# Kernel optimization log

Hardware: AMD Instinct MI355X
Metric: run time of the kernel (lower is better)

## Reference

```python
import jax, jax.numpy as jnp
import numpy as np

N_HEADS = 16
HEAD_DIM = 64
HIDDEN = N_HEADS * HEAD_DIM


def setup_inputs() -> dict:
    key = jax.random.key(0)
    ks = jax.random.split(key, 10)
    B, F, T = 2, 2048, 2048
    std = 0.02
    inp = {
        "from_tensor": jax.random.normal(ks[0], (B, F, HIDDEN), dtype=jnp.float32),
        "to_tensor": jax.random.normal(ks[1], (B, T, HIDDEN), dtype=jnp.float32),
        "attention_mask": jax.random.randint(ks[2], (B, F, T), 0, 2, dtype=jnp.int32),
        "Wq": jax.random.normal(ks[3], (HIDDEN, HIDDEN), dtype=jnp.float32) * std,
        "bq": jnp.zeros((HIDDEN,), dtype=jnp.float32),
        "Wk": jax.random.normal(ks[4], (HIDDEN, HIDDEN), dtype=jnp.float32) * std,
        "bk": jnp.zeros((HIDDEN,), dtype=jnp.float32),
        "Wv": jax.random.normal(ks[5], (HIDDEN, HIDDEN), dtype=jnp.float32) * std,
        "bv": jnp.zeros((HIDDEN,), dtype=jnp.float32),
    }
    return inp


def reference(from_tensor, to_tensor, attention_mask, Wq, bq, Wk, bk, Wv, bv):
    B, F, _ = from_tensor.shape
    T = to_tensor.shape[1]
    N, H = N_HEADS, HEAD_DIM

    # QKV projections (no activations: query/key/value act fns are None)
    q = (from_tensor @ Wq + bq).reshape(B, F, N, H)
    k = (to_tensor @ Wk + bk).reshape(B, T, N, H)
    v = (to_tensor @ Wv + bv).reshape(B, T, N, H)

    scores = jnp.einsum('BFNH,BTNH->BNFT', q, k) * (1.0 / np.sqrt(float(H)))
    # additive mask: mask [B,F,T] -> [B,1,F,T]; 0 entries get -10000
    adder = (1.0 - attention_mask.astype(jnp.float32))[:, None, :, :] * -10000.0
    scores = scores + adder
    probs = jax.nn.softmax(scores, axis=-1)  # dropout skipped (inference)

    context = jnp.einsum('BNFT,BTNH->BFNH', probs, v)
    return context.reshape(B, F, N * H)
```

## Files before the change

### kernel.cpp

```cpp
#include <hip/hip_runtime.h>


typedef short v8s __attribute__((ext_vector_type(8)));
typedef float v4f __attribute__((ext_vector_type(4)));
typedef unsigned short u16;
typedef unsigned int   u32;
typedef unsigned long long u64;

constexpr float QSCALE = 0.18033688011112042f;

__device__ __forceinline__ u16 f2bf(float f) {
    u32 u = __builtin_bit_cast(u32, f);
    u += 0x7fffu + ((u >> 16) & 1u);
    return (u16)(u >> 16);
}

__device__ __forceinline__ u32 pack_bf16(float a, float b) {
    u32 ua = __builtin_bit_cast(u32, a);
    u32 ub = __builtin_bit_cast(u32, b);
    ua += 0x7fffu + ((ua >> 16) & 1u);
    ub += 0x7fffu + ((ub >> 16) & 1u);
    return (ua >> 16) | (ub & 0xffff0000u);
}

__device__ __forceinline__ v8s ld8(const u16* p) {
    return *reinterpret_cast<const v8s*>(p);
}

__device__ __forceinline__ void async16(const void* g, void* l) {
    __builtin_amdgcn_global_load_lds(
        (const __attribute__((address_space(1))) u32*)g,
        (__attribute__((address_space(3))) u32*)l, 16, 0, 0);
}

__global__ void cvt_bf16_2(const float* __restrict__ a, const float* __restrict__ bsrc,
                           u16* __restrict__ da, u16* __restrict__ db, int n4) {
    int i = blockIdx.x * blockDim.x + threadIdx.x;
    const float4* s;
    ushort4* d;
    int j;
    if (i < n4) { s = (const float4*)a;    d = (ushort4*)da; j = i; }
    else        { s = (const float4*)bsrc; d = (ushort4*)db; j = i - n4; }
    float4 v = s[j];
    ushort4 o;
    o.x = f2bf(v.x); o.y = f2bf(v.y); o.z = f2bf(v.z); o.w = f2bf(v.w);
    d[j] = o;
}

__global__ void transpose_w(const float* __restrict__ Wq, const float* __restrict__ Wk,
                            const float* __restrict__ Wv,
                            u16* __restrict__ Wqt, u16* __restrict__ Wkt, u16* __restrict__ Wvt) {
    __shared__ float tile[32][33];
    const float* W = blockIdx.z == 0 ? Wq : (blockIdx.z == 1 ? Wk : Wv);
    u16* Wt = blockIdx.z == 0 ? Wqt : (blockIdx.z == 1 ? Wkt : Wvt);
    const int tx = threadIdx.x, ty = threadIdx.y;
    const int n0 = blockIdx.x * 32, k0 = blockIdx.y * 32;
    for (int i = 0; i < 4; i++)
        tile[ty + i * 8][tx] = W[(size_t)(k0 + ty + i * 8) * 1024 + n0 + tx];
    __syncthreads();
    for (int i = 0; i < 4; i++)
        Wt[(size_t)(n0 + ty + i * 8) * 1024 + k0 + tx] = f2bf(tile[tx][ty + i * 8]);
}

__global__ void mask_pack(const int* __restrict__ mask, u64* __restrict__ words, int nwords) {
    int g = blockIdx.x * blockDim.x + threadIdx.x;
    int w = g >> 6, lane = g & 63;
    if (w < nwords) {
        int v = mask[(size_t)w * 64 + lane];
        u64 bits = __ballot(v != 0);
        if (lane == 0) words[w] = bits;
    }
}

__global__ __launch_bounds__(256) void gemm_qkv(
    const u16* __restrict__ Xf, const u16* __restrict__ Xt,
    const u16* __restrict__ Wqt, const u16* __restrict__ Wkt, const u16* __restrict__ Wvt,
    const float* __restrict__ bq, const float* __restrict__ bk, const float* __restrict__ bv,
    u16* __restrict__ Qb, u16* __restrict__ Kb, u16* __restrict__ Vtb) {
    const int z = blockIdx.z;
    const u16* A      = z == 0 ? Xf : Xt;
    const u16* Bt     = z == 0 ? Wqt : (z == 1 ? Wkt : Wvt);
    const float* bias = z == 0 ? bq : (z == 1 ? bk : bv);
    u16* C            = z == 0 ? Qb : (z == 1 ? Kb : Vtb);
    const int mode    = (z == 2);
    const float sc    = (z == 0) ? QSCALE : 1.0f;

    __shared__ u16 As[128 * 32];
    __shared__ u16 Bs[128 * 32];
    const uint4* Ag = reinterpret_cast<const uint4*>(A);
    const uint4* Bg = reinterpret_cast<const uint4*>(Bt);

    const int tid = threadIdx.x;
    const int lane = tid & 63, wave = tid >> 6;
    const int quad = lane >> 4, l16 = lane & 15;
    const int wm = wave >> 1, wn = wave & 1;
    const int m0 = blockIdx.x * 128, n0 = blockIdx.y * 128;

    const int cg  = (lane & 3) ^ ((lane >> 3) & 3);
    const int sw8 = (quad ^ ((l16 >> 1) & 3)) * 8;

    const int r0 = (wave * 2 + 0) * 16 + (lane >> 2);
    const int r1 = (wave * 2 + 1) * 16 + (lane >> 2);
    const uint4* ap0 = Ag + (size_t)(m0 + r0) * 128 + cg;
    const uint4* ap1 = Ag + (size_t)(m0 + r1) * 128 + cg;
    const uint4* bp0 = Bg + (size_t)(n0 + r0) * 128 + cg;
    const uint4* bp1 = Bg + (size_t)(n0 + r1) * 128 + cg;

    v4f acc[4][4];
    for (int i = 0; i < 4; i++)
        for (int j = 0; j < 4; j++) acc[i][j] = (v4f)0.0f;

    for (int k0 = 0; k0 < 32; k0++) {
        __syncthreads();
        async16(ap0, As + (wave * 2 + 0) * 512); ap0 += 4;
        async16(ap1, As + (wave * 2 + 1) * 512); ap1 += 4;
        async16(bp0, Bs + (wave * 2 + 0) * 512); bp0 += 4;
        async16(bp1, Bs + (wave * 2 + 1) * 512); bp1 += 4;
        __syncthreads();

        v8s af[4], bf[4];
        #pragma unroll
        for (int mt = 0; mt < 4; mt++) af[mt] = ld8(&As[(wm * 64 + mt * 16 + l16) * 32 + sw8]);
        #pragma unroll
        for (int nt = 0; nt < 4; nt++) bf[nt] = ld8(&Bs[(wn * 64 + nt * 16 + l16) * 32 + sw8]);
        #pragma unroll
        for (int mt = 0; mt < 4; mt++)
            #pragma unroll
            for (int nt = 0; nt < 4; nt++)
                acc[mt][nt] = __builtin_amdgcn_mfma_f32_16x16x32_bf16(af[mt], bf[nt], acc[mt][nt], 0, 0, 0);
    }

    #pragma unroll
    for (int nt = 0; nt < 4; nt++) {
        const int col = n0 + wn * 64 + nt * 16 + l16;
        const float bvv = bias[col];
        #pragma unroll
        for (int mt = 0; mt < 4; mt++) {
            const int mbase = m0 + wm * 64 + mt * 16 + quad * 4;
            if (mode == 0) {
                for (int r = 0; r < 4; r++)
                    C[(size_t)(mbase + r) * 1024 + col] = f2bf((acc[mt][nt][r] + bvv) * sc);
            } else {
                const int b = mbase >> 11, t = mbase & 2047;
                const int head = col >> 6, h = col & 63;
                ushort4 pk;
                pk.x = f2bf(acc[mt][nt][0] + bvv);
                pk.y = f2bf(acc[mt][nt][1] + bvv);
                pk.z = f2bf(acc[mt][nt][2] + bvv);
                pk.w = f2bf(acc[mt][nt][3] + bvv);
                *reinterpret_cast<ushort4*>(&C[(size_t)((b * 16 + head) * 64 + h) * 2048 + t]) = pk;
            }
        }
    }
}

__global__ __launch_bounds__(256, 2) void attn_fused(
    const u16* __restrict__ Qb, const u16* __restrict__ Kb,
    const u16* __restrict__ Vtb, const u64* __restrict__ mw,
    float* __restrict__ out) {
    __shared__ u16 Ks[2][2][64][32];
    __shared__ u16 Vs[2][2][64][32];
    __shared__ u32 Ps[4][32 * 36];

    const int tid = threadIdx.x;
    const int lane = tid & 63, wave = tid >> 6;
    const int quad = lane >> 4, l16 = lane & 15;
    const int b = blockIdx.x >> 4, head = blockIdx.x & 15;
    const int f0 = blockIdx.y * 128;

    const uint4* Kg = reinterpret_cast<const uint4*>(Kb);
    const uint4* Vg = reinterpret_cast<const uint4*>(Vtb);
    const size_t vbase4 = (size_t)(b * 16 + head) * 64 * 256;

    const int cg  = (lane & 3) ^ ((lane >> 3) & 3);
    const int sw8 = (quad ^ ((l16 >> 1) & 3)) * 8;

    v8s qf[2][2];
    #pragma unroll
    for (int kk = 0; kk < 2; kk++)
        #pragma unroll
        for (int qh = 0; qh < 2; qh++)
            qf[kk][qh] = ld8(Qb + ((size_t)(b * 2048 + f0 + wave * 32 + qh * 16 + l16) * 16 + head) * 64
                                + kk * 32 + quad * 8);

    const int kr0 = ((wave * 2 + 0) * 64 + lane) >> 2;
    const int kr1 = ((wave * 2 + 1) * 64 + lane) >> 2;
    const uint4* kp0 = Kg + ((size_t)(b * 2048 + (kr0 & 63)) * 16 + head) * 8 + (kr0 >> 6) * 4 + cg;
    const uint4* kp1 = Kg + ((size_t)(b * 2048 + (kr1 & 63)) * 16 + head) * 8 + (kr1 >> 6) * 4 + cg;
    const uint4* vp0 = Vg + vbase4 + (size_t)(kr0 & 63) * 256 + (kr0 >> 6) * 4 + cg;
    const uint4* vp1 = Vg + vbase4 + (size_t)(kr1 & 63) * 256 + (kr1 >> 6) * 4 + cg;
    const int dK0 = (wave * 2 + 0) * 512, dK1 = (wave * 2 + 1) * 512;

    float lsum[2] = {0.f, 0.f};
    v4f accO[2][4];
    #pragma unroll
    for (int qh = 0; qh < 2; qh++)
        for (int ht = 0; ht < 4; ht++) accO[qh][ht] = (v4f)0.0f;

    u32* myPs = Ps[wave];
    const u64* mrow = mw + (size_t)(b * 2048 + f0 + wave * 32 + l16) * 32;

    async16(kp0, (u16*)Ks + dK0); kp0 += 8192;
    async16(kp1, (u16*)Ks + dK1); kp1 += 8192;
    async16(vp0, (u16*)Vs + dK0); vp0 += 8;
    async16(vp1, (u16*)Vs + dK1); vp1 += 8;
    __syncthreads();

    for (int it = 0; it < 32; it++) {
        const int cur = it & 1, nxt = cur ^ 1;
        if (it < 31) {
            async16(kp0, (u16*)Ks + nxt * 4096 + dK0); kp0 += 8192;
            async16(kp1, (u16*)Ks + nxt * 4096 + dK1); kp1 += 8192;
            async16(vp0, (u16*)Vs + nxt * 4096 + dK0); vp0 += 8;
            async16(vp1, (u16*)Vs + nxt * 4096 + dK1); vp1 += 8;
        }

        v4f s[2][4];
        #pragma unroll
        for (int qh = 0; qh < 2; qh++)
            for (int mt = 0; mt < 4; mt++) s[qh][mt] = (v4f)0.0f;
        #pragma unroll
        for (int kk = 0; kk < 2; kk++) {
            v8s kf[4];
            #pragma unroll
            for (int mt = 0; mt < 4; mt++) kf[mt] = ld8(&Ks[cur][kk][mt * 16 + l16][sw8]);
            #pragma unroll
            for (int qh = 0; qh < 2; qh++)
                #pragma unroll
                for (int mt = 0; mt < 4; mt++)
                    s[qh][mt] = __builtin_amdgcn_mfma_f32_16x16x32_bf16(kf[mt], qf[kk][qh], s[qh][mt], 0, 0, 0);
        }

        u32 pk[2][8];
        #pragma unroll
        for (int qh = 0; qh < 2; qh++) {
            const u64 w = mrow[qh * 512 + it];
            const u32 lo = (u32)(w >> (quad * 4));
            const u32 hi = (u32)(w >> (quad * 4 + 32));
            float sum = 0.f;
            #pragma unroll
            for (int mt = 0; mt < 4; mt++) {
                const u32 bits = ((mt & 2) ? hi : lo) >> ((mt & 1) * 16);
                float p[4];
                #pragma unroll
                for (int r = 0; r < 4; r++) {
                    const float e = __builtin_amdgcn_exp2f(s[qh][mt][r]);
                    p[r] = ((bits >> r) & 1u) ? e : 0.0f;
                    sum += p[r];
                }
                pk[qh][mt * 2]     = pack_bf16(p[0], p[1]);
                pk[qh][mt * 2 + 1] = pack_bf16(p[2], p[3]);
            }
            lsum[qh] += sum;
        }

        #pragma unroll
        for (int qh = 0; qh < 2; qh++) {
            const int row = qh * 16 + l16;
            #pragma unroll
            for (int mt = 0; mt < 4; mt++)
                *reinterpret_cast<uint2*>(&myPs[row * 36 + mt * 8 + quad * 2]) =
                    make_uint2(pk[qh][mt * 2], pk[qh][mt * 2 + 1]);
        }

        #pragma unroll
        for (int kk = 0; kk < 2; kk++) {
            v8s vf[4];
            #pragma unroll
            for (int ht = 0; ht < 4; ht++) vf[ht] = ld8(&Vs[cur][kk][ht * 16 + l16][sw8]);
            #pragma unroll
            for (int qh = 0; qh < 2; qh++) {
                const v8s pf = *reinterpret_cast<const v8s*>(
                    &myPs[(qh * 16 + l16) * 36 + kk * 16 + quad * 4]);
                #pragma unroll
                for (int ht = 0; ht < 4; ht++)
                    accO[qh][ht] = __builtin_amdgcn_mfma_f32_16x16x32_bf16(vf[ht], pf, accO[qh][ht], 0, 0, 0);
            }
        }

        __syncthreads();
    }

    #pragma unroll
    for (int qh = 0; qh < 2; qh++) {
        float l = lsum[qh];
        l += __shfl_xor(l, 16);
        l += __shfl_xor(l, 32);
        const float inv = 1.0f / l;
        const size_t ro = (size_t)(b * 2048 + f0 + wave * 32 + qh * 16 + l16) * 1024 + head * 64;
        #pragma unroll
        for (int ht = 0; ht < 4; ht++) {
            float4 o;
            o.x = accO[qh][ht][0] * inv;
            o.y = accO[qh][ht][1] * inv;
            o.z = accO[qh][ht][2] * inv;
            o.w = accO[qh][ht][3] * inv;
            *reinterpret_cast<float4*>(&out[ro + ht * 16 + quad * 4]) = o;
        }
    }
}

extern "C" void kernel_launch(void* const* d_in, const int* in_sizes, int n_in,
                              void* d_out, int out_size, void* d_ws, size_t ws_size,
                              hipStream_t stream) {
    const float* from = (const float*)d_in[0];
    const float* to   = (const float*)d_in[1];
    const int*   mask = (const int*)d_in[2];
    const float* Wq = (const float*)d_in[3];
    const float* bq = (const float*)d_in[4];
    const float* Wk = (const float*)d_in[5];
    const float* bk = (const float*)d_in[6];
    const float* Wv = (const float*)d_in[7];
    const float* bv = (const float*)d_in[8];
    float* out = (float*)d_out;

    u16* Xf  = (u16*)d_ws;
    u16* Xt  = Xf  + 4194304;
    u16* Wqt = Xt  + 4194304;
    u16* Wkt = Wqt + 1048576;
    u16* Wvt = Wkt + 1048576;
    u16* Qb  = Wvt + 1048576;
    u16* Kb  = Qb  + 4194304;
    u16* Vtb = Kb  + 4194304;
    u64* mwords = (u64*)(Vtb + 4194304);

    cvt_bf16_2<<<8192, 256, 0, stream>>>(from, to, Xf, Xt, 1048576);
    transpose_w<<<dim3(32, 32, 3), dim3(32, 8), 0, stream>>>(Wq, Wk, Wv, Wqt, Wkt, Wvt);
    mask_pack<<<32768, 256, 0, stream>>>(mask, mwords, 131072);

    gemm_qkv<<<dim3(32, 8, 3), 256, 0, stream>>>(Xf, Xt, Wqt, Wkt, Wvt, bq, bk, bv, Qb, Kb, Vtb);

    attn_fused<<<dim3(32, 16), 256, 0, stream>>>(Qb, Kb, Vtb, mwords, out);
}
```

Measured before the change: 251.6 us.

## Split attention over two key halves, merge prep kernels, add reduction pass

Merges the three preprocessing kernels into one launch. The attention kernel now splits the key dimension into two halves across a grid z-dimension, which doubles the block count, and raises launch bounds to 4 blocks per CU. It does this by dropping double buffering to a single buffer with two syncs per iteration. Row sums are computed with an extra MFMA against a ones vector instead of scalar adds, and P is truncated rather than rounded to bf16. A new reduce kernel combines the two partial outputs, reusing workspace for the second half (it overwrites the Xf/Xt staging buffers and the transposed weights). This adds extra global traffic and loses load/compute overlap.

```diff
diff --git a/kernel.cpp b/kernel.cpp
--- a/kernel.cpp
+++ b/kernel.cpp
@@ -15,11 +15,9 @@
     return (u16)(u >> 16);
 }
 
-__device__ __forceinline__ u32 pack_bf16(float a, float b) {
+__device__ __forceinline__ u32 pack_trunc(float a, float b) {
     u32 ua = __builtin_bit_cast(u32, a);
     u32 ub = __builtin_bit_cast(u32, b);
-    ua += 0x7fffu + ((ua >> 16) & 1u);
-    ub += 0x7fffu + ((ub >> 16) & 1u);
     return (ua >> 16) | (ub & 0xffff0000u);
 }
 
@@ -33,39 +31,40 @@
         (__attribute__((address_space(3))) u32*)l, 16, 0, 0);
 }
 
-__global__ void cvt_bf16_2(const float* __restrict__ a, const float* __restrict__ bsrc,
-                           u16* __restrict__ da, u16* __restrict__ db, int n4) {
-    int i = blockIdx.x * blockDim.x + threadIdx.x;
-    const float4* s;
-    ushort4* d;
-    int j;
-    if (i < n4) { s = (const float4*)a;    d = (ushort4*)da; j = i; }
-    else        { s = (const float4*)bsrc; d = (ushort4*)db; j = i - n4; }
-    float4 v = s[j];
-    ushort4 o;
-    o.x = f2bf(v.x); o.y = f2bf(v.y); o.z = f2bf(v.z); o.w = f2bf(v.w);
-    d[j] = o;
-}
-
-__global__ void transpose_w(const float* __restrict__ Wq, const float* __restrict__ Wk,
-                            const float* __restrict__ Wv,
-                            u16* __restrict__ Wqt, u16* __restrict__ Wkt, u16* __restrict__ Wvt) {
+__global__ __launch_bounds__(256) void prep(
+    const float* __restrict__ from, const float* __restrict__ to,
+    u16* __restrict__ Xf, u16* __restrict__ Xt,
+    const float* __restrict__ Wq, const float* __restrict__ Wk, const float* __restrict__ Wv,
+    u16* __restrict__ Wqt, u16* __restrict__ Wkt, u16* __restrict__ Wvt,
+    const int* __restrict__ mask, u64* __restrict__ words) {
     __shared__ float tile[32][33];
-    const float* W = blockIdx.z == 0 ? Wq : (blockIdx.z == 1 ? Wk : Wv);
-    u16* Wt = blockIdx.z == 0 ? Wqt : (blockIdx.z == 1 ? Wkt : Wvt);
-    const int tx = threadIdx.x, ty = threadIdx.y;
-    const int n0 = blockIdx.x * 32, k0 = blockIdx.y * 32;
-    for (int i = 0; i < 4; i++)
-        tile[ty + i * 8][tx] = W[(size_t)(k0 + ty + i * 8) * 1024 + n0 + tx];
-    __syncthreads();
-    for (int i = 0; i < 4; i++)
-        Wt[(size_t)(n0 + ty + i * 8) * 1024 + k0 + tx] = f2bf(tile[tx][ty + i * 8]);
-}
-
-__global__ void mask_pack(const int* __restrict__ mask, u64* __restrict__ words, int nwords) {
-    int g = blockIdx.x * blockDim.x + threadIdx.x;
-    int w = g >> 6, lane = g & 63;
-    if (w < nwords) {
+    const int bid = blockIdx.x, tid = threadIdx.x;
+    if (bid < 8192) {
+        int i = bid * 256 + tid;
+        const float4* s;
+        ushort4* d;
+        int j;
+        if (i < 1048576) { s = (const float4*)from; d = (ushort4*)Xf; j = i; }
+        else             { s = (const float4*)to;   d = (ushort4*)Xt; j = i - 1048576; }
+        float4 v = s[j];
+        ushort4 o;
+        o.x = f2bf(v.x); o.y = f2bf(v.y); o.z = f2bf(v.z); o.w = f2bf(v.w);
+        d[j] = o;
+    } else if (bid < 11264) {
+        const int r = bid - 8192;
+        const int zz = r >> 10, rem = r & 1023;
+        const float* W = zz == 0 ? Wq : (zz == 1 ? Wk : Wv);
+        u16* Wt = zz == 0 ? Wqt : (zz == 1 ? Wkt : Wvt);
+        const int tx = tid & 31, ty = tid >> 5;
+        const int n0 = (rem & 31) * 32, k0 = (rem >> 5) * 32;
+        for (int i = 0; i < 4; i++)
+            tile[ty + i * 8][tx] = W[(size_t)(k0 + ty + i * 8) * 1024 + n0 + tx];
+        __syncthreads();
+        for (int i = 0; i < 4; i++)
+            Wt[(size_t)(n0 + ty + i * 8) * 1024 + k0 + tx] = f2bf(tile[tx][ty + i * 8]);
+    } else {
+        int g = (bid - 11264) * 256 + tid;
+        int w = g >> 6, lane = g & 63;
         int v = mask[(size_t)w * 64 + lane];
         u64 bits = __ballot(v != 0);
         if (lane == 0) words[w] = bits;
@@ -154,12 +153,13 @@
     }
 }
 
-__global__ __launch_bounds__(256, 2) void attn_fused(
+__global__ __launch_bounds__(256, 4) void attn_fused(
     const u16* __restrict__ Qb, const u16* __restrict__ Kb,
     const u16* __restrict__ Vtb, const u64* __restrict__ mw,
-    float* __restrict__ out) {
-    __shared__ u16 Ks[2][2][64][32];
-    __shared__ u16 Vs[2][2][64][32];
+    float* __restrict__ out, float* __restrict__ O1,
+    float* __restrict__ l0w, float* __restrict__ l1w) {
+    __shared__ u16 Ks[2][64][32];
+    __shared__ u16 Vs[2][64][32];
     __shared__ u32 Ps[4][32 * 36];
 
     const int tid = threadIdx.x;
@@ -167,6 +167,8 @@
     const int quad = lane >> 4, l16 = lane & 15;
     const int b = blockIdx.x >> 4, head = blockIdx.x & 15;
     const int f0 = blockIdx.y * 128;
+    const int thalf = blockIdx.z;
+    const int tbase = thalf * 1024;
 
     const uint4* Kg = reinterpret_cast<const uint4*>(Kb);
     const uint4* Vg = reinterpret_cast<const uint4*>(Vtb);
@@ -183,37 +185,35 @@
             qf[kk][qh] = ld8(Qb + ((size_t)(b * 2048 + f0 + wave * 32 + qh * 16 + l16) * 16 + head) * 64
                                 + kk * 32 + quad * 8);
 
+    v8s ones;
+    #pragma unroll
+    for (int i = 0; i < 8; i++) ones[i] = (short)0x3F80;
+
     const int kr0 = ((wave * 2 + 0) * 64 + lane) >> 2;
     const int kr1 = ((wave * 2 + 1) * 64 + lane) >> 2;
-    const uint4* kp0 = Kg + ((size_t)(b * 2048 + (kr0 & 63)) * 16 + head) * 8 + (kr0 >> 6) * 4 + cg;
-    const uint4* kp1 = Kg + ((size_t)(b * 2048 + (kr1 & 63)) * 16 + head) * 8 + (kr1 >> 6) * 4 + cg;
-    const uint4* vp0 = Vg + vbase4 + (size_t)(kr0 & 63) * 256 + (kr0 >> 6) * 4 + cg;
-    const uint4* vp1 = Vg + vbase4 + (size_t)(kr1 & 63) * 256 + (kr1 >> 6) * 4 + cg;
+    const uint4* kp0 = Kg + ((size_t)(b * 2048 + tbase + (kr0 & 63)) * 16 + head) * 8 + (kr0 >> 6) * 4 + cg;
+    const uint4* kp1 = Kg + ((size_t)(b * 2048 + tbase + (kr1 & 63)) * 16 + head) * 8 + (kr1 >> 6) * 4 + cg;
+    const uint4* vp0 = Vg + vbase4 + (size_t)(kr0 & 63) * 256 + (tbase >> 3) + (kr0 >> 6) * 4 + cg;
+    const uint4* vp1 = Vg + vbase4 + (size_t)(kr1 & 63) * 256 + (tbase >> 3) + (kr1 >> 6) * 4 + cg;
     const int dK0 = (wave * 2 + 0) * 512, dK1 = (wave * 2 + 1) * 512;
 
-    float lsum[2] = {0.f, 0.f};
-    v4f accO[2][4];
-    #pragma unroll
-    for (int qh = 0; qh < 2; qh++)
+    v4f accO[2][4], accL[2];
+    #pragma unroll
+    for (int qh = 0; qh < 2; qh++) {
+        accL[qh] = (v4f)0.0f;
         for (int ht = 0; ht < 4; ht++) accO[qh][ht] = (v4f)0.0f;
+    }
 
     u32* myPs = Ps[wave];
-    const u64* mrow = mw + (size_t)(b * 2048 + f0 + wave * 32 + l16) * 32;
-
-    async16(kp0, (u16*)Ks + dK0); kp0 += 8192;
-    async16(kp1, (u16*)Ks + dK1); kp1 += 8192;
-    async16(vp0, (u16*)Vs + dK0); vp0 += 8;
-    async16(vp1, (u16*)Vs + dK1); vp1 += 8;
-    __syncthreads();
-
-    for (int it = 0; it < 32; it++) {
-        const int cur = it & 1, nxt = cur ^ 1;
-        if (it < 31) {
-            async16(kp0, (u16*)Ks + nxt * 4096 + dK0); kp0 += 8192;
-            async16(kp1, (u16*)Ks + nxt * 4096 + dK1); kp1 += 8192;
-            async16(vp0, (u16*)Vs + nxt * 4096 + dK0); vp0 += 8;
-            async16(vp1, (u16*)Vs + nxt * 4096 + dK1); vp1 += 8;
-        }
+    const u64* mrow = mw + (size_t)(b * 2048 + f0 + wave * 32 + l16) * 32 + thalf * 16;
+
+    for (int it = 0; it < 16; it++) {
+        __syncthreads();
+        async16(kp0, (u16*)Ks + dK0); kp0 += 8192;
+        async16(kp1, (u16*)Ks + dK1); kp1 += 8192;
+        async16(vp0, (u16*)Vs + dK0); vp0 += 8;
+        async16(vp1, (u16*)Vs + dK1); vp1 += 8;
+        __syncthreads();
 
         v4f s[2][4];
         #pragma unroll
@@ -223,7 +223,7 @@
         for (int kk = 0; kk < 2; kk++) {
             v8s kf[4];
             #pragma unroll
-            for (int mt = 0; mt < 4; mt++) kf[mt] = ld8(&Ks[cur][kk][mt * 16 + l16][sw8]);
+            for (int mt = 0; mt < 4; mt++) kf[mt] = ld8(&Ks[kk][mt * 16 + l16][sw8]);
             #pragma unroll
             for (int qh = 0; qh < 2; qh++)
                 #pragma unroll
@@ -237,7 +237,6 @@
             const u64 w = mrow[qh * 512 + it];
             const u32 lo = (u32)(w >> (quad * 4));
             const u32 hi = (u32)(w >> (quad * 4 + 32));
-            float sum = 0.f;
             #pragma unroll
             for (int mt = 0; mt < 4; mt++) {
                 const u32 bits = ((mt & 2) ? hi : lo) >> ((mt & 1) * 16);
@@ -246,12 +245,10 @@
                 for (int r = 0; r < 4; r++) {
                     const float e = __builtin_amdgcn_exp2f(s[qh][mt][r]);
                     p[r] = ((bits >> r) & 1u) ? e : 0.0f;
-                    sum += p[r];
                 }
-                pk[qh][mt * 2]     = pack_bf16(p[0], p[1]);
-                pk[qh][mt * 2 + 1] = pack_bf16(p[2], p[3]);
+                pk[qh][mt * 2]     = pack_trunc(p[0], p[1]);
+                pk[qh][mt * 2 + 1] = pack_trunc(p[2], p[3]);
             }
-            lsum[qh] += sum;
         }
 
         #pragma unroll
@@ -267,7 +264,7 @@
         for (int kk = 0; kk < 2; kk++) {
             v8s vf[4];
             #pragma unroll
-            for (int ht = 0; ht < 4; ht++) vf[ht] = ld8(&Vs[cur][kk][ht * 16 + l16][sw8]);
+            for (int ht = 0; ht < 4; ht++) vf[ht] = ld8(&Vs[kk][ht * 16 + l16][sw8]);
             #pragma unroll
             for (int qh = 0; qh < 2; qh++) {
                 const v8s pf = *reinterpret_cast<const v8s*>(
@@ -275,29 +272,39 @@
                 #pragma unroll
                 for (int ht = 0; ht < 4; ht++)
                     accO[qh][ht] = __builtin_amdgcn_mfma_f32_16x16x32_bf16(vf[ht], pf, accO[qh][ht], 0, 0, 0);
+                accL[qh] = __builtin_amdgcn_mfma_f32_16x16x32_bf16(ones, pf, accL[qh], 0, 0, 0);
             }
         }
-
-        __syncthreads();
-    }
-
+    }
+
+    float* dst = thalf ? O1 : out;
+    float* lws = thalf ? l1w : l0w;
     #pragma unroll
     for (int qh = 0; qh < 2; qh++) {
-        float l = lsum[qh];
-        l += __shfl_xor(l, 16);
-        l += __shfl_xor(l, 32);
-        const float inv = 1.0f / l;
-        const size_t ro = (size_t)(b * 2048 + f0 + wave * 32 + qh * 16 + l16) * 1024 + head * 64;
-        #pragma unroll
-        for (int ht = 0; ht < 4; ht++) {
-            float4 o;
-            o.x = accO[qh][ht][0] * inv;
-            o.y = accO[qh][ht][1] * inv;
-            o.z = accO[qh][ht][2] * inv;
-            o.w = accO[qh][ht][3] * inv;
-            *reinterpret_cast<float4*>(&out[ro + ht * 16 + quad * 4]) = o;
-        }
-    }
+        const int row = b * 2048 + f0 + wave * 32 + qh * 16 + l16;
+        if (quad == 0) lws[(size_t)row * 16 + head] = accL[qh][0];
+        const size_t ro = (size_t)row * 1024 + head * 64;
+        #pragma unroll
+        for (int ht = 0; ht < 4; ht++)
+            *reinterpret_cast<float4*>(&dst[ro + ht * 16 + quad * 4]) =
+                *reinterpret_cast<float4*>(&accO[qh][ht]);
+    }
+}
+
+__global__ __launch_bounds__(256) void reduce_out(
+    float* __restrict__ out, const float* __restrict__ O1,
+    const float* __restrict__ l0w, const float* __restrict__ l1w) {
+    const int i4 = blockIdx.x * 256 + threadIdx.x;
+    const int flat = i4 * 4;
+    const int row = flat >> 10, head = (flat >> 6) & 15;
+    float4 a = reinterpret_cast<float4*>(out)[i4];
+    const float4 c = reinterpret_cast<const float4*>(O1)[i4];
+    const float inv = 1.0f / (l0w[row * 16 + head] + l1w[row * 16 + head]);
+    a.x = (a.x + c.x) * inv;
+    a.y = (a.y + c.y) * inv;
+    a.z = (a.z + c.z) * inv;
+    a.w = (a.w + c.w) * inv;
+    reinterpret_cast<float4*>(out)[i4] = a;
 }
 
 extern "C" void kernel_launch(void* const* d_in, const int* in_sizes, int n_in,
@@ -324,11 +331,15 @@
     u16* Vtb = Kb  + 4194304;
     u64* mwords = (u64*)(Vtb + 4194304);
 
-    cvt_bf16_2<<<8192, 256, 0, stream>>>(from, to, Xf, Xt, 1048576);
-    transpose_w<<<dim3(32, 32, 3), dim3(32, 8), 0, stream>>>(Wq, Wk, Wv, Wqt, Wkt, Wvt);
-    mask_pack<<<32768, 256, 0, stream>>>(mask, mwords, 131072);
+    float* O1  = (float*)d_ws;
+    float* l0w = (float*)Wqt;
+    float* l1w = l0w + 65536;
+
+    prep<<<44032, 256, 0, stream>>>(from, to, Xf, Xt, Wq, Wk, Wv, Wqt, Wkt, Wvt, mask, mwords);
 
     gemm_qkv<<<dim3(32, 8, 3), 256, 0, stream>>>(Xf, Xt, Wqt, Wkt, Wvt, bq, bk, bv, Qb, Kb, Vtb);
 
-    attn_fused<<<dim3(32, 16), 256, 0, stream>>>(Qb, Kb, Vtb, mwords, out);
-}
+    attn_fused<<<dim3(32, 16, 2), 256, 0, stream>>>(Qb, Kb, Vtb, mwords, out, O1, l0w, l1w);
+
+    reduce_out<<<4096, 256, 0, stream>>>(out, O1, l0w, l1w);
+}
```

Measured after the change: 238.0 us. 5.4% less time.
